# Optimization experiments

Measured on AMD Instinct MI355X. Metric: run time of the kernel, lower is better.

The kernel has to match this reference:

```python
import jax, jax.numpy as jnp
import numpy as np

D_MODEL = 2048
N_HEADS = 16
HEAD_DIM = D_MODEL // N_HEADS


def setup_inputs() -> dict:
    key = jax.random.key(0)
    ks = jax.random.split(key, 5)
    s = 0.02
    return {
        "x": jax.random.normal(ks[0], (4, 2048, D_MODEL), dtype=jnp.float32),
        "w_qkv": jax.random.normal(ks[1], (D_MODEL, 3 * D_MODEL), dtype=jnp.float32) * s,
        "b_qkv": jnp.zeros((3 * D_MODEL,), dtype=jnp.float32),
        "w_out": jax.random.normal(ks[2], (D_MODEL, D_MODEL), dtype=jnp.float32) * s,
        "b_out": jnp.zeros((D_MODEL,), dtype=jnp.float32),
    }


def reference(x, w_qkv, b_qkv, w_out, b_out):
    B, T, C = x.shape
    qkv = x @ w_qkv + b_qkv  # [B,T,3C]
    q, k, v = jnp.split(qkv, 3, axis=-1)
    # [B,T,C] -> [B,H,T,hd]
    def to_heads(t):
        return t.reshape(B, T, N_HEADS, HEAD_DIM).transpose(0, 2, 1, 3)
    q, k, v = to_heads(q), to_heads(k), to_heads(v)
    scale = 1.0 / jnp.sqrt(jnp.asarray(HEAD_DIM, dtype=x.dtype))
    attn = jnp.einsum("bhqd,bhkd->bhqk", q, k) * scale
    causal = jnp.tril(jnp.ones((T, T), dtype=bool))
    attn = jnp.where(causal[None, None], attn, jnp.asarray(-jnp.inf, dtype=attn.dtype))
    attn = jax.nn.softmax(attn, axis=-1)
    out = jnp.einsum("bhqk,bhkd->bhqd", attn, v)
    out = out.transpose(0, 2, 1, 3).reshape(B, T, C)
    return out @ w_out + b_out
```

## Files before the change

kernel.cpp:

```cpp
#include <hip/hip_runtime.h>
#include <hip/hip_bf16.h>

#define DEVFN static __device__ __forceinline__

typedef __attribute__((ext_vector_type(8))) __bf16 bf16x8;
typedef __attribute__((ext_vector_type(4))) float f32x4;

#define MFMA16(a, b, c) __builtin_amdgcn_mfma_f32_16x16x32_bf16(a, b, c, 0, 0, 0)

DEVFN void gload16(const void* g, void* l) {
  __builtin_amdgcn_global_load_lds((const __attribute__((address_space(1))) void*)g,
                                   (__attribute__((address_space(3))) void*)l, 16, 0, 0);
}

DEVFN void vwait8() { asm volatile("s_waitcnt vmcnt(8)" ::: "memory"); __builtin_amdgcn_sched_barrier(0); }
DEVFN void vwait4() { asm volatile("s_waitcnt vmcnt(4)" ::: "memory"); __builtin_amdgcn_sched_barrier(0); }
DEVFN void vwait0() { asm volatile("s_waitcnt vmcnt(0)" ::: "memory"); __builtin_amdgcn_sched_barrier(0); }
DEVFN void lgk0()   { asm volatile("s_waitcnt lgkmcnt(0)" ::: "memory"); __builtin_amdgcn_sched_barrier(0); }
DEVFN void bar()    { __builtin_amdgcn_s_barrier(); }
DEVFN void barsched() { __builtin_amdgcn_s_barrier(); __builtin_amdgcn_sched_barrier(0); }

__global__ __launch_bounds__(256) void cvt_f32_bf16(const float* __restrict__ in,
                                                    __bf16* __restrict__ out) {
  size_t i = ((size_t)blockIdx.x * 256 + threadIdx.x) * 8;
  f32x4 a = *(const f32x4*)(in + i);
  f32x4 b = *(const f32x4*)(in + i + 4);
  bf16x8 u;
  u[0] = (__bf16)a[0]; u[1] = (__bf16)a[1]; u[2] = (__bf16)a[2]; u[3] = (__bf16)a[3];
  u[4] = (__bf16)b[0]; u[5] = (__bf16)b[1]; u[6] = (__bf16)b[2]; u[7] = (__bf16)b[3];
  *(bf16x8*)(out + i) = u;
}

__global__ __launch_bounds__(256) void transpose_w(const float* __restrict__ in,
                                                   __bf16* __restrict__ out,
                                                   int K, int N) {
  __shared__ float tile[32][33];
  const int t = threadIdx.x, tx = t & 31, ty = t >> 5;
  const int n0 = blockIdx.x * 32, k0 = blockIdx.y * 32;
#pragma unroll
  for (int r = 0; r < 4; r++)
    tile[ty + r * 8][tx] = in[(size_t)(k0 + ty + r * 8) * N + n0 + tx];
  __syncthreads();
#pragma unroll
  for (int r = 0; r < 4; r++)
    out[(size_t)(n0 + ty + r * 8) * K + k0 + tx] = (__bf16)tile[tx][ty + r * 8];
}

__global__ __launch_bounds__(256) void transpose_v(const __bf16* __restrict__ in,
                                                   __bf16* __restrict__ out) {
  __shared__ __bf16 tile[64][72];
  const int bh = blockIdx.z;
  const int t0 = blockIdx.x * 64, d0 = blockIdx.y * 64;
  const int tid = threadIdx.x;
  const int r = tid >> 3, c8 = (tid & 7) * 8;
  const __bf16* ip = in + (size_t)bh * 2048 * 128;
#pragma unroll
  for (int i = 0; i < 2; i++)
    *(bf16x8*)&tile[i * 32 + r][c8] =
        *(const bf16x8*)(ip + (size_t)(t0 + i * 32 + r) * 128 + d0 + c8);
  __syncthreads();
  __bf16* op = out + (size_t)bh * 2048 * 128;
#pragma unroll
  for (int i = 0; i < 2; i++) {
    const int dd = i * 32 + r;
    bf16x8 v;
#pragma unroll
    for (int j = 0; j < 8; j++) v[j] = tile[c8 + j][dd];
    *(bf16x8*)(op + (size_t)(d0 + dd) * 2048 + t0 + c8) = v;
  }
}

#define QK_SCALE 0.12751745f

DEVFN void stage_tile(const __bf16* gx, size_t Kst, int t, __bf16* ldst,
                      int rr, int gsw, int w) {
#pragma unroll
  for (int j = 0; j < 4; j++)
    gload16(gx + (size_t)(j * 64 + rr) * Kst + (size_t)t * 64 + gsw,
            ldst + j * 4096 + w * 512);
}

DEVFN void tile_step(__bf16* la, __bf16* lb, f32x4 (&acc)[8][4],
                     const __bf16* ga, const __bf16* gb, size_t Kst, int t, int NT,
                     int rr, int gsw, int w, int wr, int wc, int lg, int li) {
  bf16x8 a[4][2], bl[2][2], br[2][2];
  const int sa = li & 7;
  const int arow = wr * 128 + li;
  const int brow = wc * 64 + li;

#pragma unroll
  for (int mi = 0; mi < 4; mi++)
#pragma unroll
    for (int ks = 0; ks < 2; ks++)
      a[mi][ks] = *(const bf16x8*)&la[(arow + mi * 16) * 64 + (((ks * 4 + lg) ^ sa) * 8)];
#pragma unroll
  for (int ni = 0; ni < 2; ni++)
#pragma unroll
    for (int ks = 0; ks < 2; ks++)
      bl[ni][ks] = *(const bf16x8*)&lb[(brow + ni * 16) * 64 + (((ks * 4 + lg) ^ sa) * 8)];
  bar();
  lgk0();
  __builtin_amdgcn_s_setprio(1);
#pragma unroll
  for (int mi = 0; mi < 4; mi++)
#pragma unroll
    for (int ni = 0; ni < 2; ni++)
#pragma unroll
      for (int ks = 0; ks < 2; ks++)
        acc[mi][ni] = MFMA16(a[mi][ks], bl[ni][ks], acc[mi][ni]);
  __builtin_amdgcn_s_setprio(0);
  bar();

#pragma unroll
  for (int ni = 0; ni < 2; ni++)
#pragma unroll
    for (int ks = 0; ks < 2; ks++)
      br[ni][ks] = *(const bf16x8*)&lb[(brow + (ni + 2) * 16) * 64 + (((ks * 4 + lg) ^ sa) * 8)];
  bar();
  lgk0();
  __builtin_amdgcn_s_setprio(1);
#pragma unroll
  for (int mi = 0; mi < 4; mi++)
#pragma unroll
    for (int ni = 0; ni < 2; ni++)
#pragma unroll
      for (int ks = 0; ks < 2; ks++)
        acc[mi][ni + 2] = MFMA16(a[mi][ks], br[ni][ks], acc[mi][ni + 2]);
  __builtin_amdgcn_s_setprio(0);
  bar();

#pragma unroll
  for (int mi = 0; mi < 4; mi++)
#pragma unroll
    for (int ks = 0; ks < 2; ks++)
      a[mi][ks] = *(const bf16x8*)&la[(arow + (mi + 4) * 16) * 64 + (((ks * 4 + lg) ^ sa) * 8)];
  bar();
  lgk0();
  __builtin_amdgcn_s_setprio(1);
#pragma unroll
  for (int mi = 0; mi < 4; mi++)
#pragma unroll
    for (int ni = 0; ni < 2; ni++)
#pragma unroll
      for (int ks = 0; ks < 2; ks++)
        acc[mi + 4][ni] = MFMA16(a[mi][ks], bl[ni][ks], acc[mi + 4][ni]);
  __builtin_amdgcn_s_setprio(0);
  bar();

  if (t + 2 < NT) {
    stage_tile(ga, Kst, t + 2, la, rr, gsw, w);
    stage_tile(gb, Kst, t + 2, lb, rr, gsw, w);
  }
  __builtin_amdgcn_s_setprio(1);
#pragma unroll
  for (int mi = 0; mi < 4; mi++)
#pragma unroll
    for (int ni = 0; ni < 2; ni++)
#pragma unroll
      for (int ks = 0; ks < 2; ks++)
        acc[mi + 4][ni + 2] = MFMA16(a[mi][ks], br[ni][ks], acc[mi + 4][ni + 2]);
  __builtin_amdgcn_s_setprio(0);

  if (t + 2 < NT) vwait8(); else vwait0();
  bar();
}

template <int MODE>
__global__ __launch_bounds__(512, 2) void gemm256(
    const __bf16* __restrict__ A, const __bf16* __restrict__ Bt,
    const float* __restrict__ bias, int K, int Ncols,
    __bf16* __restrict__ qo, __bf16* __restrict__ ko, __bf16* __restrict__ vo,
    float* __restrict__ outf) {
  __shared__ __align__(16) __bf16 lds[65536];
  const int tid = threadIdx.x;
  const int w = tid >> 6, lane = tid & 63;
  const int wr = w >> 2, wc = w & 3;
  const int lg = lane >> 4, li = lane & 15;
  const size_t m0 = (size_t)blockIdx.y * 256;
  const size_t n0 = (size_t)blockIdx.x * 256;
  const int rr = tid >> 3;
  const int gsw = ((tid & 7) ^ (rr & 7)) * 8;
  const __bf16* ga = A + m0 * K;
  const __bf16* gb = Bt + n0 * K;
  const int NT = K >> 6;

  __bf16* la0 = lds;
  __bf16* la1 = lds + 16384;
  __bf16* lb0 = lds + 32768;
  __bf16* lb1 = lds + 49152;

  f32x4 acc[8][4] = {};

  stage_tile(ga, K, 0, la0, rr, gsw, w);
  stage_tile(gb, K, 0, lb0, rr, gsw, w);
  stage_tile(ga, K, 1, la1, rr, gsw, w);
  stage_tile(gb, K, 1, lb1, rr, gsw, w);
  vwait8();
  bar();

  for (int t = 0; t < NT; t += 2) {
    tile_step(la0, lb0, acc, ga, gb, K, t,     NT, rr, gsw, w, wr, wc, lg, li);
    tile_step(la1, lb1, acc, ga, gb, K, t + 1, NT, rr, gsw, w, wr, wc, lg, li);
  }

  if (MODE == 0) {
    const int which = (int)(n0 >> 11);
    const int b = (int)(m0 >> 11);
    __bf16* outp = (which == 0) ? qo : ((which == 1) ? ko : vo);
    const float scale = (which == 0) ? QK_SCALE : 1.0f;
#pragma unroll
    for (int ni = 0; ni < 4; ni++) {
      const int ncol = (int)n0 + wc * 64 + ni * 16 + li;
      const float bv = bias[ncol];
      const int h = (ncol & 2047) >> 7;
      const int d = ncol & 127;
      const size_t base = (size_t)(b * 16 + h) * (2048 * 128) + d;
#pragma unroll
      for (int mi = 0; mi < 8; mi++)
#pragma unroll
        for (int r = 0; r < 4; r++) {
          const int tt = ((int)m0 + wr * 128 + mi * 16 + lg * 4 + r) & 2047;
          outp[base + (size_t)tt * 128] = (__bf16)((acc[mi][ni][r] + bv) * scale);
        }
    }
  } else {
#pragma unroll
    for (int ni = 0; ni < 4; ni++) {
      const int ncol = (int)n0 + wc * 64 + ni * 16 + li;
      const float bv = bias[ncol];
#pragma unroll
      for (int mi = 0; mi < 8; mi++)
#pragma unroll
        for (int r = 0; r < 4; r++) {
          const size_t mrow = m0 + wr * 128 + mi * 16 + lg * 4 + r;
          outf[mrow * Ncols + ncol] = acc[mi][ni][r] + bv;
        }
    }
  }
}

DEVFN void attn_stageK(const __bf16* const (&ksrc)[4], int k0, __bf16* Kl, int w) {
#pragma unroll
  for (int i = 0; i < 4; i++)
    gload16(ksrc[i] + (size_t)k0 * 128, Kl + i * 2048 + w * 512);
}
DEVFN void attn_stageV(const __bf16* const (&vsrc)[4], int k0, __bf16* Vl, int w) {
#pragma unroll
  for (int i = 0; i < 4; i++)
    gload16(vsrc[i] + k0, Vl + i * 2048 + w * 512);
}

template <bool DIAG>
DEVFN void attn_tile(int kt, int n, int q0, int w, int lg, int li,
                     const __bf16* const (&ksrc)[4], const __bf16* const (&vsrc)[4],
                     __bf16* Kl, __bf16* Vl, __bf16* Pl,
                     const bf16x8 (&qf)[2][4], f32x4 (&o)[2][8],
                     float (&mrow)[2][4], float (&lrow)[2][4]) {
  const int k0 = kt * 64;
  const bool more = (kt + 1 < n);

  vwait4();
  barsched();

  f32x4 s[2][4] = {};
#pragma unroll
  for (int kk = 0; kk < 4; kk++) {
    bf16x8 bk[4];
#pragma unroll
    for (int ni = 0; ni < 4; ni++) {
      const int key = ni * 16 + li;
      bk[ni] = *(const bf16x8*)&Kl[key * 128 + ((kk * 32 + lg * 8) ^ ((key & 7) << 3))];
    }
#pragma unroll
    for (int mi = 0; mi < 2; mi++)
#pragma unroll
      for (int ni = 0; ni < 4; ni++)
        s[mi][ni] = MFMA16(qf[mi][kk], bk[ni], s[mi][ni]);
  }
  barsched();
  if (more) attn_stageK(ksrc, k0 + 64, Kl, w);

#pragma unroll
  for (int mi = 0; mi < 2; mi++) {
#pragma unroll
    for (int r = 0; r < 4; r++) {
      const int prow = w * 32 + mi * 16 + lg * 4 + r;
      float vals[4];
#pragma unroll
      for (int ni = 0; ni < 4; ni++) {
        float x = s[mi][ni][r];
        if (DIAG) {
          if ((k0 + ni * 16 + li) > (q0 + prow)) x = -1e30f;
        }
        vals[ni] = x;
      }
      float vmax = fmaxf(fmaxf(vals[0], vals[1]), fmaxf(vals[2], vals[3]));
      vmax = fmaxf(vmax, __shfl_xor(vmax, 1));
      vmax = fmaxf(vmax, __shfl_xor(vmax, 2));
      vmax = fmaxf(vmax, __shfl_xor(vmax, 4));
      vmax = fmaxf(vmax, __shfl_xor(vmax, 8));
      float mref = mrow[mi][r];
      if (vmax - mref > 8.0f) {
        const float sc = __builtin_amdgcn_exp2f(mref - vmax);
        lrow[mi][r] *= sc;
#pragma unroll
        for (int nd = 0; nd < 8; nd++) o[mi][nd][r] *= sc;
        mrow[mi][r] = vmax;
        mref = vmax;
      }
      float ps = 0.f;
#pragma unroll
      for (int ni = 0; ni < 4; ni++) {
        const float p = __builtin_amdgcn_exp2f(vals[ni] - mref);
        ps += p;
        Pl[prow * 72 + ni * 16 + li] = (__bf16)p;
      }
      ps += __shfl_xor(ps, 1);
      ps += __shfl_xor(ps, 2);
      ps += __shfl_xor(ps, 4);
      ps += __shfl_xor(ps, 8);
      lrow[mi][r] += ps;
    }
  }

  if (more) vwait4(); else vwait0();
  barsched();

#pragma unroll
  for (int kk = 0; kk < 2; kk++) {
    bf16x8 pf[2];
#pragma unroll
    for (int mi = 0; mi < 2; mi++)
      pf[mi] = *(const bf16x8*)&Pl[(w * 32 + mi * 16 + li) * 72 + kk * 32 + lg * 8];
#pragma unroll
    for (int nd = 0; nd < 8; nd++) {
      const int d = nd * 16 + li;
      const int swd = ((d ^ (d >> 3)) & 7) << 3;
      bf16x8 vf = *(const bf16x8*)&Vl[d * 64 + ((kk * 32 + lg * 8) ^ swd)];
#pragma unroll
      for (int mi = 0; mi < 2; mi++)
        o[mi][nd] = MFMA16(pf[mi], vf, o[mi][nd]);
    }
  }
  barsched();
  if (more) attn_stageV(vsrc, k0 + 64, Vl, w);
}

DEVFN void attn_run(int qt, int bh, int w, int lg, int li,
                    const __bf16* qp, __bf16* ob,
                    const __bf16* const (&ksrc)[4], const __bf16* const (&vsrc)[4],
                    __bf16* Kl, __bf16* Vl, __bf16* Pl) {
  const int q0 = qt * 128;
  bf16x8 qf[2][4];
#pragma unroll
  for (int mi = 0; mi < 2; mi++)
#pragma unroll
    for (int kk = 0; kk < 4; kk++)
      qf[mi][kk] = *(const bf16x8*)(qp + (size_t)(q0 + w * 32 + mi * 16 + li) * 128 + kk * 32 + lg * 8);

  f32x4 o[2][8] = {};
  float mrow[2][4], lrow[2][4];
#pragma unroll
  for (int mi = 0; mi < 2; mi++)
#pragma unroll
    for (int r = 0; r < 4; r++) { mrow[mi][r] = -1e30f; lrow[mi][r] = 0.f; }

  const int n = 2 * qt + 2;
  attn_stageK(ksrc, 0, Kl, w);
  attn_stageV(vsrc, 0, Vl, w);

  for (int kt = 0; kt < n - 2; kt++)
    attn_tile<false>(kt, n, q0, w, lg, li, ksrc, vsrc, Kl, Vl, Pl, qf, o, mrow, lrow);
  attn_tile<true>(n - 2, n, q0, w, lg, li, ksrc, vsrc, Kl, Vl, Pl, qf, o, mrow, lrow);
  attn_tile<true>(n - 1, n, q0, w, lg, li, ksrc, vsrc, Kl, Vl, Pl, qf, o, mrow, lrow);

  const int b = bh >> 4, h = bh & 15;
#pragma unroll
  for (int mi = 0; mi < 2; mi++) {
    float inv[4];
#pragma unroll
    for (int r = 0; r < 4; r++) inv[r] = 1.0f / lrow[mi][r];
#pragma unroll
    for (int nd = 0; nd < 8; nd++)
#pragma unroll
      for (int r = 0; r < 4; r++)
        ob[(size_t)(b * 2048 + q0 + w * 32 + mi * 16 + lg * 4 + r) * 2048 + h * 128 + nd * 16 + li]
            = (__bf16)(o[mi][nd][r] * inv[r]);
  }
}

__global__ __launch_bounds__(256, 2) void attn_fwd(
    const __bf16* __restrict__ qb, const __bf16* __restrict__ kb,
    const __bf16* __restrict__ vtb, __bf16* __restrict__ ob) {
  __shared__ __align__(16) __bf16 Kl[64 * 128];
  __shared__ __align__(16) __bf16 Vl[128 * 64];
  __shared__ __align__(16) __bf16 Pl[128 * 72];
  const int bx = blockIdx.x;
  const int bh = blockIdx.y;
  const int tid = threadIdx.x;
  const int w = tid >> 6, l = tid & 63;
  const int lg = l >> 4, li = l & 15;
  const __bf16* qp = qb + (size_t)bh * (2048 * 128);
  const __bf16* kp = kb + (size_t)bh * (2048 * 128);
  const __bf16* vtp = vtb + (size_t)bh * (2048 * 128);

  const __bf16* ksrc[4];
  const __bf16* vsrc[4];
#pragma unroll
  for (int i = 0; i < 4; i++) {
    const int key = i * 16 + w * 4 + lg;
    ksrc[i] = kp + (size_t)key * 128 + 8 * (li ^ (key & 7));
    const int d = i * 32 + (tid >> 3);
    const int g = (tid & 7) ^ ((d ^ (d >> 3)) & 7);
    vsrc[i] = vtp + (size_t)d * 2048 + g * 8;
  }

  attn_run(15 - bx, bh, w, lg, li, qp, ob, ksrc, vsrc, Kl, Vl, Pl);
  attn_run(bx,      bh, w, lg, li, qp, ob, ksrc, vsrc, Kl, Vl, Pl);
}

extern "C" void kernel_launch(void* const* d_in, const int* in_sizes, int n_in,
                              void* d_out, int out_size, void* d_ws, size_t ws_size,
                              hipStream_t stream) {
  (void)in_sizes; (void)n_in; (void)out_size; (void)ws_size;
  const float* x     = (const float*)d_in[0];
  const float* w_qkv = (const float*)d_in[1];
  const float* b_qkv = (const float*)d_in[2];
  const float* w_out = (const float*)d_in[3];
  const float* b_out = (const float*)d_in[4];
  float* out = (float*)d_out;
  char* ws = (char*)d_ws;

  __bf16* xb    = (__bf16*)(ws + 0);
  __bf16* wqkvT = (__bf16*)(ws + 33554432);
  __bf16* qbuf  = (__bf16*)(ws + 58720256);
  __bf16* kbuf  = (__bf16*)(ws + 92274688);
  __bf16* vbuf  = (__bf16*)(ws + 125829120);
  __bf16* woutT = (__bf16*)(ws + 159383552);

  cvt_f32_bf16<<<8192, 256, 0, stream>>>(x, xb);
  transpose_w<<<dim3(192, 64), 256, 0, stream>>>(w_qkv, wqkvT, 2048, 6144);
  transpose_w<<<dim3(64, 64), 256, 0, stream>>>(w_out, woutT, 2048, 2048);
  gemm256<0><<<dim3(24, 32), 512, 0, stream>>>(xb, wqkvT, b_qkv, 2048, 6144,
                                               qbuf, kbuf, vbuf, nullptr);
  transpose_v<<<dim3(32, 2, 64), 256, 0, stream>>>(vbuf, xb);
  attn_fwd<<<dim3(8, 64), 256, 0, stream>>>(qbuf, kbuf, xb, vbuf);
  gemm256<1><<<dim3(8, 32), 512, 0, stream>>>(vbuf, woutT, b_out, 2048, 2048,
                                              nullptr, nullptr, nullptr, out);
}
```

Measured before the change: 470.1 us.

## Split GEMM prefetch earlier, drop LDS waits, add XCD-aware block swizzle

In the GEMM tile step, the next B tile is now prefetched after the second MFMA phase and the next A tile after the third, rather than both at the end. The explicit lgkmcnt(0) waits after the barriers are removed, leaving LDS-read dependencies to the compiler. Both the GEMM and attention kernels remap block IDs with an (orig&7)-based swizzle so consecutive blocks on the same XCD share operand tiles in L2. Issuing the B prefetch earlier overwrites lb while later phases still read br from registers, which relies on the barrier ordering being correct.

After: 452.5 us. -3.7%, faster.

```diff
diff --git a/kernel.cpp b/kernel.cpp
--- a/kernel.cpp
+++ b/kernel.cpp
@@ -16,7 +16,6 @@
 DEVFN void vwait8() { asm volatile("s_waitcnt vmcnt(8)" ::: "memory"); __builtin_amdgcn_sched_barrier(0); }
 DEVFN void vwait4() { asm volatile("s_waitcnt vmcnt(4)" ::: "memory"); __builtin_amdgcn_sched_barrier(0); }
 DEVFN void vwait0() { asm volatile("s_waitcnt vmcnt(0)" ::: "memory"); __builtin_amdgcn_sched_barrier(0); }
-DEVFN void lgk0()   { asm volatile("s_waitcnt lgkmcnt(0)" ::: "memory"); __builtin_amdgcn_sched_barrier(0); }
 DEVFN void bar()    { __builtin_amdgcn_s_barrier(); }
 DEVFN void barsched() { __builtin_amdgcn_s_barrier(); __builtin_amdgcn_sched_barrier(0); }
 
@@ -87,6 +86,7 @@
   const int sa = li & 7;
   const int arow = wr * 128 + li;
   const int brow = wc * 64 + li;
+  const bool pf = (t + 2 < NT);
 
 #pragma unroll
   for (int mi = 0; mi < 4; mi++)
@@ -99,7 +99,6 @@
     for (int ks = 0; ks < 2; ks++)
       bl[ni][ks] = *(const bf16x8*)&lb[(brow + ni * 16) * 64 + (((ks * 4 + lg) ^ sa) * 8)];
   bar();
-  lgk0();
   __builtin_amdgcn_s_setprio(1);
 #pragma unroll
   for (int mi = 0; mi < 4; mi++)
@@ -117,7 +116,6 @@
     for (int ks = 0; ks < 2; ks++)
       br[ni][ks] = *(const bf16x8*)&lb[(brow + (ni + 2) * 16) * 64 + (((ks * 4 + lg) ^ sa) * 8)];
   bar();
-  lgk0();
   __builtin_amdgcn_s_setprio(1);
 #pragma unroll
   for (int mi = 0; mi < 4; mi++)
@@ -127,15 +125,15 @@
       for (int ks = 0; ks < 2; ks++)
         acc[mi][ni + 2] = MFMA16(a[mi][ks], br[ni][ks], acc[mi][ni + 2]);
   __builtin_amdgcn_s_setprio(0);
-  bar();
-
+  barsched();
+
+  if (pf) stage_tile(gb, Kst, t + 2, lb, rr, gsw, w);
 #pragma unroll
   for (int mi = 0; mi < 4; mi++)
 #pragma unroll
     for (int ks = 0; ks < 2; ks++)
       a[mi][ks] = *(const bf16x8*)&la[(arow + (mi + 4) * 16) * 64 + (((ks * 4 + lg) ^ sa) * 8)];
   bar();
-  lgk0();
   __builtin_amdgcn_s_setprio(1);
 #pragma unroll
   for (int mi = 0; mi < 4; mi++)
@@ -145,12 +143,9 @@
       for (int ks = 0; ks < 2; ks++)
         acc[mi + 4][ni] = MFMA16(a[mi][ks], bl[ni][ks], acc[mi + 4][ni]);
   __builtin_amdgcn_s_setprio(0);
-  bar();
-
-  if (t + 2 < NT) {
-    stage_tile(ga, Kst, t + 2, la, rr, gsw, w);
-    stage_tile(gb, Kst, t + 2, lb, rr, gsw, w);
-  }
+  barsched();
+
+  if (pf) stage_tile(ga, Kst, t + 2, la, rr, gsw, w);
   __builtin_amdgcn_s_setprio(1);
 #pragma unroll
   for (int mi = 0; mi < 4; mi++)
@@ -161,7 +156,7 @@
         acc[mi + 4][ni + 2] = MFMA16(a[mi][ks], br[ni][ks], acc[mi + 4][ni + 2]);
   __builtin_amdgcn_s_setprio(0);
 
-  if (t + 2 < NT) vwait8(); else vwait0();
+  if (pf) vwait8(); else vwait0();
   bar();
 }
 
@@ -176,8 +171,12 @@
   const int w = tid >> 6, lane = tid & 63;
   const int wr = w >> 2, wc = w & 3;
   const int lg = lane >> 4, li = lane & 15;
-  const size_t m0 = (size_t)blockIdx.y * 256;
-  const size_t n0 = (size_t)blockIdx.x * 256;
+  const int nbx = gridDim.x;
+  const int nwg = nbx * gridDim.y;
+  const int orig = blockIdx.y * nbx + blockIdx.x;
+  const int swz = (orig & 7) * (nwg >> 3) + (orig >> 3);
+  const size_t m0 = (size_t)(swz / nbx) * 256;
+  const size_t n0 = (size_t)(swz % nbx) * 256;
   const int rr = tid >> 3;
   const int gsw = ((tid & 7) ^ (rr & 7)) * 8;
   const __bf16* ga = A + m0 * K;
@@ -395,8 +394,10 @@
   __shared__ __align__(16) __bf16 Kl[64 * 128];
   __shared__ __align__(16) __bf16 Vl[128 * 64];
   __shared__ __align__(16) __bf16 Pl[128 * 72];
-  const int bx = blockIdx.x;
-  const int bh = blockIdx.y;
+  const int orig = (int)blockIdx.y * 8 + (int)blockIdx.x;
+  const int swz = (orig & 7) * 64 + (orig >> 3);
+  const int bx = swz & 7;
+  const int bh = swz >> 3;
   const int tid = threadIdx.x;
   const int w = tid >> 6, l = tid & 63;
   const int lg = l >> 4, li = l & 15;
```
